# Kernel optimization log

Hardware: AMD Instinct MI355X
Metric: run time of the kernel (lower is better)

## Reference

```python
import jax, jax.numpy as jnp
import numpy as np

N = 100000
E = 800000
D = 128


def setup_inputs() -> dict:
    key = jax.random.key(0)
    k1, k2, k3, k4 = jax.random.split(key, 4)
    x = jax.random.normal(k1, (N, D), dtype=jnp.float32)
    edge_index = jax.random.randint(k2, (2, E), 0, N, dtype=jnp.int64)
    s = 1.0 / np.sqrt(D)
    W1 = jax.random.uniform(k3, (D, D), jnp.float32, -s, s)
    b1 = jnp.zeros((D,), jnp.float32)
    W2 = jax.random.uniform(k4, (D, D), jnp.float32, -s, s)
    b2 = jnp.zeros((D,), jnp.float32)
    return {"x": x, "edge_index": edge_index, "W1": W1, "b1": b1, "W2": W2, "b2": b2}


def _degree(idx, n, dtype):
    return jax.ops.segment_sum(jnp.ones(idx.shape, dtype), idx, num_segments=n)


def _graph_conv(x, row, col, W, b, residual, act):
    n = x.shape[0]
    deg_out = jnp.clip(_degree(row, n, x.dtype), 1.0)          # [N]
    x_src = x * jax.lax.rsqrt(deg_out)[:, None]                # [N, D]
    # scatter-add messages from source (row) into target (col)
    agg = jax.ops.segment_sum(x_src[row], col, num_segments=n)  # [N, D]
    out = agg @ W.T + b
    deg_in = jnp.clip(_degree(col, n, x.dtype), 1.0)
    out = out * jax.lax.rsqrt(deg_in)[:, None]
    if residual:
        out = out + x  # res_fc is Identity (in_dim == out_dim)
    if act:
        out = jax.nn.relu(out)
    return out


def reference(x, edge_index, W1, b1, W2, b2):
    row, col = edge_index[0], edge_index[1]
    # layer 1: relu + residual; layer 2 (last, encoding=False): no act, no residual
    h = _graph_conv(x, row, col, W1, b1, residual=True, act=True)
    h = _graph_conv(h, row, col, W2, b2, residual=False, act=False)
    return h
```

## Files before the change

kernel.cpp:

```cpp
#include <hip/hip_runtime.h>


#define NN 100000
#define EE 800000
#define DD 128
#define NB1 98
#define CB  3125
#define XB  12500
#define NTILE (NN / 16)

typedef __attribute__((ext_vector_type(8))) short short8;
typedef __attribute__((ext_vector_type(4))) float floatx4;

__device__ inline float bf2f(unsigned int u16) {
    union { unsigned int i; float f; } c;
    c.i = u16 << 16;
    return c.f;
}
__device__ inline ushort f2bf(float f) {
    union { float f; unsigned int i; } c;
    c.f = f;
    unsigned int u = c.i;
    return (ushort)((u + 0x7fffu + ((u >> 16) & 1u)) >> 16);
}

__global__ __launch_bounds__(256) void countcast_kernel(const int* __restrict__ row,
                                                        const int* __restrict__ col,
                                                        int* __restrict__ cnt_out,
                                                        int* __restrict__ cnt_in,
                                                        int* __restrict__ off,
                                                        const float* __restrict__ x,
                                                        ushort* __restrict__ xb) {
    const int b = blockIdx.x;
    if (b < CB) {
        int e = b * 256 + threadIdx.x;
        off[e] = atomicAdd(&cnt_in[col[e]], 1);
        atomicAdd(&cnt_out[row[e]], 1);
    } else {
        int idx = (b - CB) * 256 + threadIdx.x;
        float4 v = ((const float4*)x)[idx];
        ushort4 o;
        o.x = f2bf(v.x); o.y = f2bf(v.y); o.z = f2bf(v.z); o.w = f2bf(v.w);
        ((ushort4*)xb)[idx] = o;
    }
}

__global__ __launch_bounds__(256) void scan1_kernel(const int* __restrict__ cnt,
                                                    int* __restrict__ excl,
                                                    int* __restrict__ bsums) {
    __shared__ int tmp[256];
    const int t = threadIdx.x;
    const int base = blockIdx.x * 1024 + t * 4;
    int a[4];
#pragma unroll
    for (int q = 0; q < 4; ++q) a[q] = (base + q < NN) ? cnt[base + q] : 0;
    int s = a[0] + a[1] + a[2] + a[3];
    tmp[t] = s;
    __syncthreads();
    for (int off = 1; off < 256; off <<= 1) {
        int v = 0;
        if (t >= off) v = tmp[t - off];
        __syncthreads();
        tmp[t] += v;
        __syncthreads();
    }
    int excl_s = tmp[t] - s;
    if (t == 255) bsums[blockIdx.x] = tmp[t];
    int run = excl_s;
#pragma unroll
    for (int q = 0; q < 4; ++q) {
        if (base + q < NN) excl[base + q] = run;
        run += a[q];
    }
}

__global__ __launch_bounds__(256) void scanB_kernel(const int* __restrict__ excl,
                                                    const int* __restrict__ bsums,
                                                    const int* __restrict__ cnt_out,
                                                    const int* __restrict__ cnt_in,
                                                    int* __restrict__ row_start,
                                                    float* __restrict__ dinv_out,
                                                    float* __restrict__ dinv_in) {
    __shared__ int tmp[128];
    const int t = threadIdx.x;
    if (t < 128) tmp[t] = (t < NB1) ? bsums[t] : 0;
    __syncthreads();
    for (int off = 1; off < 128; off <<= 1) {
        int v = 0;
        if (t < 128 && t >= off) v = tmp[t - off];
        __syncthreads();
        if (t < 128) tmp[t] += v;
        __syncthreads();
    }
    const int base = (blockIdx.x == 0) ? 0 : tmp[blockIdx.x - 1];
    const int i0 = blockIdx.x * 1024 + t * 4;
#pragma unroll
    for (int q = 0; q < 4; ++q) {
        int i = i0 + q;
        if (i < NN) {
            row_start[i] = excl[i] + base;
            dinv_in[i]  = rsqrtf((float)max(cnt_in[i], 1));
            dinv_out[i] = rsqrtf((float)max(cnt_out[i], 1));
        }
    }
    if (blockIdx.x == 0 && t == 0) row_start[NN] = EE;
}

__global__ __launch_bounds__(256) void fill_kernel(const int* __restrict__ row,
                                                   const int* __restrict__ col,
                                                   const int* __restrict__ row_start,
                                                   const int* __restrict__ off,
                                                   int* __restrict__ srcs) {
    int e = blockIdx.x * 256 + threadIdx.x;
    if (e < EE) srcs[row_start[col[e]] + off[e]] = row[e];
}

__global__ __launch_bounds__(256) void gather_kernel(const ushort* __restrict__ src,
                                                     const int* __restrict__ row_start,
                                                     const int* __restrict__ srcs,
                                                     const float* __restrict__ dinv_out,
                                                     ushort* __restrict__ agg) {
    const int node = blockIdx.x * 16 + (threadIdx.x >> 4);
    const int lane = threadIdx.x & 15;
    if (node >= NN) return;
    int p = row_start[node];
    const int end = row_start[node + 1];
    float a0 = 0.f, a1 = 0.f, a2 = 0.f, a3 = 0.f;
    float a4 = 0.f, a5 = 0.f, a6 = 0.f, a7 = 0.f;

#define ACCUM(V, C)                                  \
    do {                                             \
        a0 += bf2f((V).x & 0xffffu) * (C);           \
        a1 += bf2f((V).x >> 16) * (C);               \
        a2 += bf2f((V).y & 0xffffu) * (C);           \
        a3 += bf2f((V).y >> 16) * (C);               \
        a4 += bf2f((V).z & 0xffffu) * (C);           \
        a5 += bf2f((V).z >> 16) * (C);               \
        a6 += bf2f((V).w & 0xffffu) * (C);           \
        a7 += bf2f((V).w >> 16) * (C);               \
    } while (0)

    for (; p + 3 < end; p += 4) {
        int s0 = srcs[p];
        int s1 = srcs[p + 1];
        int s2 = srcs[p + 2];
        int s3 = srcs[p + 3];
        float c0 = dinv_out[s0];
        float c1 = dinv_out[s1];
        float c2 = dinv_out[s2];
        float c3 = dinv_out[s3];
        uint4 v0 = ((const uint4*)(src + (size_t)s0 * DD))[lane];
        uint4 v1 = ((const uint4*)(src + (size_t)s1 * DD))[lane];
        uint4 v2 = ((const uint4*)(src + (size_t)s2 * DD))[lane];
        uint4 v3 = ((const uint4*)(src + (size_t)s3 * DD))[lane];
        ACCUM(v0, c0); ACCUM(v1, c1); ACCUM(v2, c2); ACCUM(v3, c3);
    }
    for (; p < end; ++p) {
        int s0 = srcs[p];
        float c0 = dinv_out[s0];
        uint4 v0 = ((const uint4*)(src + (size_t)s0 * DD))[lane];
        ACCUM(v0, c0);
    }
#undef ACCUM

    uint4 o;
    o.x = (unsigned int)f2bf(a0) | ((unsigned int)f2bf(a1) << 16);
    o.y = (unsigned int)f2bf(a2) | ((unsigned int)f2bf(a3) << 16);
    o.z = (unsigned int)f2bf(a4) | ((unsigned int)f2bf(a5) << 16);
    o.w = (unsigned int)f2bf(a6) | ((unsigned int)f2bf(a7) << 16);
    ((uint4*)(agg + (size_t)node * DD))[lane] = o;
}

template <bool L1>
__global__ __launch_bounds__(256) void gemm_ep(const ushort* __restrict__ agg,
                                               const float* __restrict__ W,
                                               const float* __restrict__ bias,
                                               const float* __restrict__ dinv_in,
                                               const float* __restrict__ x,
                                               ushort* __restrict__ hb,
                                               float* __restrict__ out) {
    __shared__ ushort Ws[128 * 136];
    {
        int j = threadIdx.x >> 1;
        int k0 = (threadIdx.x & 1) * 64;
        const float4* wp = (const float4*)(W + (size_t)j * DD + k0);
        ushort* dst = Ws + j * 136 + k0;
#pragma unroll
        for (int q = 0; q < 16; ++q) {
            float4 v = wp[q];
            ushort4 o;
            o.x = f2bf(v.x); o.y = f2bf(v.y); o.z = f2bf(v.z); o.w = f2bf(v.w);
            *(ushort4*)(dst + q * 4) = o;
        }
    }
    __syncthreads();

    const int wave = threadIdx.x >> 6;
    const int lane = threadIdx.x & 63;
    const int tile = blockIdx.x * 4 + wave;
    if (tile >= NTILE) return;
    const int mi = lane & 15;
    const int quad = lane >> 4;
    const int m0 = tile * 16;

    floatx4 acc[8];
#pragma unroll
    for (int t = 0; t < 8; ++t) acc[t] = (floatx4){0.f, 0.f, 0.f, 0.f};

    const ushort* ap = agg + (size_t)(m0 + mi) * DD + quad * 8;
#pragma unroll
    for (int s = 0; s < 4; ++s) {
        short8 a = *(const short8*)(ap + s * 32);
#pragma unroll
        for (int t = 0; t < 8; ++t) {
            short8 b = *(const short8*)(Ws + (t * 16 + mi) * 136 + s * 32 + quad * 8);
            acc[t] = __builtin_amdgcn_mfma_f32_16x16x32_bf16(a, b, acc[t], 0, 0, 0);
        }
    }

    float dv[4];
#pragma unroll
    for (int i = 0; i < 4; ++i) dv[i] = dinv_in[m0 + quad * 4 + i];
#pragma unroll
    for (int t = 0; t < 8; ++t) {
        int c = t * 16 + mi;
        float bv = bias[c];
#pragma unroll
        for (int i = 0; i < 4; ++i) {
            int r = m0 + quad * 4 + i;
            float o = (acc[t][i] + bv) * dv[i];
            if (L1) {
                o += x[(size_t)r * DD + c];
                o = fmaxf(o, 0.f);
                hb[(size_t)r * DD + c] = f2bf(o);
            } else {
                out[(size_t)r * DD + c] = o;
            }
        }
    }
}

extern "C" void kernel_launch(void* const* d_in, const int* in_sizes, int n_in,
                              void* d_out, int out_size, void* d_ws, size_t ws_size,
                              hipStream_t stream) {
    const float* x  = (const float*)d_in[0];
    const int*   ei = (const int*)d_in[1];
    const float* W1 = (const float*)d_in[2];
    const float* b1 = (const float*)d_in[3];
    const float* W2 = (const float*)d_in[4];
    const float* b2 = (const float*)d_in[5];
    float* out = (float*)d_out;

    const int* row = ei;
    const int* col = ei + EE;

    ushort* agg     = (ushort*)d_ws;
    ushort* xb      = agg + (size_t)NN * DD;
    ushort* hb      = xb;
    int*    off     = (int*)agg;
    float* dinv_out = (float*)(xb + (size_t)NN * DD);
    float* dinv_in  = dinv_out + NN;
    int*   cnt      = (int*)(dinv_in + NN);
    int*   excl     = cnt + 2 * NN;
    int*   row_st   = excl + NN;
    int*   srcs     = row_st + NN + 1;
    int*   bsums    = srcs + EE;

    hipMemsetAsync(cnt, 0, 2 * NN * sizeof(int), stream);
    countcast_kernel<<<CB + XB, 256, 0, stream>>>(row, col, cnt, cnt + NN, off, x, xb);
    scan1_kernel<<<NB1, 256, 0, stream>>>(cnt + NN, excl, bsums);
    scanB_kernel<<<NB1, 256, 0, stream>>>(excl, bsums, cnt, cnt + NN, row_st,
                                          dinv_out, dinv_in);
    fill_kernel<<<(EE + 255) / 256, 256, 0, stream>>>(row, col, row_st, off, srcs);

    gather_kernel<<<(NN + 15) / 16, 256, 0, stream>>>(xb, row_st, srcs, dinv_out, agg);
    gemm_ep<true><<<(NTILE + 3) / 4, 256, 0, stream>>>(agg, W1, b1, dinv_in, x, hb, nullptr);

    gather_kernel<<<(NN + 15) / 16, 256, 0, stream>>>(hb, row_st, srcs, dinv_out, agg);
    gemm_ep<false><<<(NTILE + 3) / 4, 256, 0, stream>>>(agg, W2, b2, dinv_in, nullptr, nullptr, out);
}
```

Measured before the change: 316.7 us.

## Build CSR via shared-memory per-chunk histograms instead of global atomics

Replaces the global-atomic degree counting and offset-based fill with a two-level scheme. Edges are split into 16 chunks and nodes into 8 ranges, each block building an LDS histogram of its range that is written out per chunk. A reduce/scan then derives degrees and per-chunk base offsets, and the fill kernel uses LDS atomics to place sources. This removes the memset and the contended global atomics, but every block rereads its whole edge chunk for each node range and the per-chunk histogram arrays add traffic. Within each chunk the edge order in the CSR is no longer deterministic.

Measured after the change: 397.7 us. +25.6%, slower.

```diff
diff --git a/kernel.cpp b/kernel.cpp
--- a/kernel.cpp
+++ b/kernel.cpp
@@ -5,8 +5,10 @@
 #define EE 800000
 #define DD 128
 #define NB1 98
-#define CB  3125
-#define XB  12500
+#define RC 16
+#define CHUNK 50000
+#define NR 8
+#define RSZ 12500
 #define NTILE (NN / 16)
 
 typedef __attribute__((ext_vector_type(8))) short short8;
@@ -24,36 +26,72 @@
     return (ushort)((u + 0x7fffu + ((u >> 16) & 1u)) >> 16);
 }
 
-__global__ __launch_bounds__(256) void countcast_kernel(const int* __restrict__ row,
-                                                        const int* __restrict__ col,
-                                                        int* __restrict__ cnt_out,
-                                                        int* __restrict__ cnt_in,
-                                                        int* __restrict__ off,
-                                                        const float* __restrict__ x,
-                                                        ushort* __restrict__ xb) {
+__global__ __launch_bounds__(256) void bighist_kernel(const int* __restrict__ row,
+                                                      const int* __restrict__ col,
+                                                      unsigned* __restrict__ H,
+                                                      unsigned* __restrict__ H2,
+                                                      const float* __restrict__ x,
+                                                      ushort* __restrict__ xb) {
+    __shared__ unsigned hist[RSZ];
     const int b = blockIdx.x;
-    if (b < CB) {
-        int e = b * 256 + threadIdx.x;
-        off[e] = atomicAdd(&cnt_in[col[e]], 1);
-        atomicAdd(&cnt_out[row[e]], 1);
+    const int t = threadIdx.x;
+    if (b < 2 * NR * RC) {
+        const int hb = b & (NR * RC - 1);
+        const int r = hb >> 4;
+        const int c = hb & (RC - 1);
+        const int* key = (b < NR * RC) ? col : row;
+        unsigned* Hd = (b < NR * RC) ? H : H2;
+        const unsigned rbase = (unsigned)(r * RSZ);
+        for (int i = t; i < RSZ; i += 256) hist[i] = 0u;
+        __syncthreads();
+        const int e0 = c * CHUNK;
+        for (int i = t; i < CHUNK; i += 256) {
+            unsigned u = (unsigned)key[e0 + i] - rbase;
+            if (u < RSZ) atomicAdd(&hist[u], 1u);
+        }
+        __syncthreads();
+        unsigned* dst = Hd + (size_t)c * NN + rbase;
+        for (int i = t; i < RSZ; i += 256) dst[i] = hist[i];
     } else {
-        int idx = (b - CB) * 256 + threadIdx.x;
-        float4 v = ((const float4*)x)[idx];
-        ushort4 o;
-        o.x = f2bf(v.x); o.y = f2bf(v.y); o.z = f2bf(v.z); o.w = f2bf(v.w);
-        ((ushort4*)xb)[idx] = o;
-    }
-}
-
-__global__ __launch_bounds__(256) void scan1_kernel(const int* __restrict__ cnt,
-                                                    int* __restrict__ excl,
-                                                    int* __restrict__ bsums) {
+        int idx = (b - 2 * NR * RC) * 256 + t;
+        if (idx < NN * 32) {
+            float4 v = ((const float4*)x)[idx];
+            ushort4 o;
+            o.x = f2bf(v.x); o.y = f2bf(v.y); o.z = f2bf(v.z); o.w = f2bf(v.w);
+            ((ushort4*)xb)[idx] = o;
+        }
+    }
+}
+
+__global__ __launch_bounds__(256) void reduceB_kernel(const unsigned* __restrict__ H,
+                                                      const unsigned* __restrict__ H2,
+                                                      int* __restrict__ excl,
+                                                      int* __restrict__ bsums,
+                                                      float* __restrict__ dinv_out,
+                                                      float* __restrict__ dinv_in) {
     __shared__ int tmp[256];
     const int t = threadIdx.x;
     const int base = blockIdx.x * 1024 + t * 4;
-    int a[4];
-#pragma unroll
-    for (int q = 0; q < 4; ++q) a[q] = (base + q < NN) ? cnt[base + q] : 0;
+    int a[4] = {0, 0, 0, 0};
+    int o[4] = {0, 0, 0, 0};
+    for (int c = 0; c < RC; ++c) {
+        const unsigned* hc  = H  + (size_t)c * NN;
+        const unsigned* h2c = H2 + (size_t)c * NN;
+#pragma unroll
+        for (int q = 0; q < 4; ++q) {
+            if (base + q < NN) {
+                a[q] += (int)hc[base + q];
+                o[q] += (int)h2c[base + q];
+            }
+        }
+    }
+#pragma unroll
+    for (int q = 0; q < 4; ++q) {
+        if (base + q < NN) {
+            dinv_in[base + q]  = rsqrtf((float)max(a[q], 1));
+            dinv_out[base + q] = rsqrtf((float)max(o[q], 1));
+        }
+    }
     int s = a[0] + a[1] + a[2] + a[3];
     tmp[t] = s;
     __syncthreads();
@@ -76,11 +114,9 @@
 
 __global__ __launch_bounds__(256) void scanB_kernel(const int* __restrict__ excl,
                                                     const int* __restrict__ bsums,
-                                                    const int* __restrict__ cnt_out,
-                                                    const int* __restrict__ cnt_in,
+                                                    const unsigned* __restrict__ H,
                                                     int* __restrict__ row_start,
-                                                    float* __restrict__ dinv_out,
-                                                    float* __restrict__ dinv_in) {
+                                                    int* __restrict__ base) {
     __shared__ int tmp[128];
     const int t = threadIdx.x;
     if (t < 128) tmp[t] = (t < NB1) ? bsums[t] : 0;
@@ -92,27 +128,46 @@
         if (t < 128) tmp[t] += v;
         __syncthreads();
     }
-    const int base = (blockIdx.x == 0) ? 0 : tmp[blockIdx.x - 1];
+    const int pfx = (blockIdx.x == 0) ? 0 : tmp[blockIdx.x - 1];
     const int i0 = blockIdx.x * 1024 + t * 4;
 #pragma unroll
     for (int q = 0; q < 4; ++q) {
         int i = i0 + q;
         if (i < NN) {
-            row_start[i] = excl[i] + base;
-            dinv_in[i]  = rsqrtf((float)max(cnt_in[i], 1));
-            dinv_out[i] = rsqrtf((float)max(cnt_out[i], 1));
+            int rs = excl[i] + pfx;
+            row_start[i] = rs;
+            int run = rs;
+            for (int c = 0; c < RC; ++c) {
+                size_t idx = (size_t)c * NN + i;
+                base[idx] = run;
+                run += (int)H[idx];
+            }
         }
     }
     if (blockIdx.x == 0 && t == 0) row_start[NN] = EE;
 }
 
-__global__ __launch_bounds__(256) void fill_kernel(const int* __restrict__ row,
-                                                   const int* __restrict__ col,
-                                                   const int* __restrict__ row_start,
-                                                   const int* __restrict__ off,
-                                                   int* __restrict__ srcs) {
-    int e = blockIdx.x * 256 + threadIdx.x;
-    if (e < EE) srcs[row_start[col[e]] + off[e]] = row[e];
+__global__ __launch_bounds__(256) void fillC_kernel(const int* __restrict__ row,
+                                                    const int* __restrict__ col,
+                                                    const int* __restrict__ base,
+                                                    int* __restrict__ srcs) {
+    __shared__ unsigned cur[RSZ];
+    const int r = blockIdx.x >> 4;
+    const int c = blockIdx.x & (RC - 1);
+    const unsigned rbase = (unsigned)(r * RSZ);
+    const int* bc = base + (size_t)c * NN + rbase;
+    for (int i = threadIdx.x; i < RSZ; i += 256) cur[i] = (unsigned)bc[i];
+    __syncthreads();
+    const int e0 = c * CHUNK;
+    for (int i = threadIdx.x; i < CHUNK; i += 256) {
+        int e = e0 + i;
+        unsigned u = (unsigned)col[e] - rbase;
+        int rv = row[e];
+        if (u < RSZ) {
+            unsigned slot = atomicAdd(&cur[u], 1u);
+            srcs[slot] = rv;
+        }
+    }
 }
 
 __global__ __launch_bounds__(256) void gather_kernel(const ushort* __restrict__ src,
@@ -254,24 +309,24 @@
     const int* row = ei;
     const int* col = ei + EE;
 
-    ushort* agg     = (ushort*)d_ws;
-    ushort* xb      = agg + (size_t)NN * DD;
+    ushort* xb      = (ushort*)d_ws;
+    ushort* agg     = xb + (size_t)NN * DD;
+    unsigned* H     = (unsigned*)agg;
+    unsigned* H2    = H + (size_t)RC * NN;
+    int*    basec   = (int*)H2;
     ushort* hb      = xb;
-    int*    off     = (int*)agg;
-    float* dinv_out = (float*)(xb + (size_t)NN * DD);
+    float* dinv_out = (float*)(agg + (size_t)NN * DD);
     float* dinv_in  = dinv_out + NN;
-    int*   cnt      = (int*)(dinv_in + NN);
-    int*   excl     = cnt + 2 * NN;
+    int*   excl     = (int*)(dinv_in + NN);
     int*   row_st   = excl + NN;
     int*   srcs     = row_st + NN + 1;
     int*   bsums    = srcs + EE;
 
-    hipMemsetAsync(cnt, 0, 2 * NN * sizeof(int), stream);
-    countcast_kernel<<<CB + XB, 256, 0, stream>>>(row, col, cnt, cnt + NN, off, x, xb);
-    scan1_kernel<<<NB1, 256, 0, stream>>>(cnt + NN, excl, bsums);
-    scanB_kernel<<<NB1, 256, 0, stream>>>(excl, bsums, cnt, cnt + NN, row_st,
-                                          dinv_out, dinv_in);
-    fill_kernel<<<(EE + 255) / 256, 256, 0, stream>>>(row, col, row_st, off, srcs);
+    bighist_kernel<<<2 * NR * RC + (NN * 32 + 255) / 256, 256, 0, stream>>>(
+        row, col, H, H2, x, xb);
+    reduceB_kernel<<<NB1, 256, 0, stream>>>(H, H2, excl, bsums, dinv_out, dinv_in);
+    scanB_kernel<<<NB1, 256, 0, stream>>>(excl, bsums, H, row_st, basec);
+    fillC_kernel<<<NR * RC, 256, 0, stream>>>(row, col, basec, srcs);
 
     gather_kernel<<<(NN + 15) / 16, 256, 0, stream>>>(xb, row_st, srcs, dinv_out, agg);
     gemm_ep<true><<<(NTILE + 3) / 4, 256, 0, stream>>>(agg, W1, b1, dinv_in, x, hb, nullptr);
```
